# Kernel tuning notes

Hardware: AMD Instinct MI355X
Metric: run time of the kernel (lower is better)

The kernel has to match this reference:

```python
import jax, jax.numpy as jnp
import numpy as np

B, T, U = 4, 256, 128
EH, PH, JH, V = 1024, 640, 640, 1024


def setup_inputs() -> dict:
    key = jax.random.key(0)
    ks = jax.random.split(key, 8)
    s_e = 1.0 / np.sqrt(EH)
    s_p = 1.0 / np.sqrt(PH)
    s_j = 1.0 / np.sqrt(JH)
    return {
        "enc": jax.random.normal(ks[0], (B, EH, T), jnp.float32),
        "dec": jax.random.normal(ks[1], (B, PH, U), jnp.float32),
        "W_enc": jax.random.uniform(ks[2], (JH, EH), jnp.float32, -s_e, s_e),
        "b_enc": jax.random.uniform(ks[3], (JH,), jnp.float32, -s_e, s_e),
        "W_pred": jax.random.uniform(ks[4], (JH, PH), jnp.float32, -s_p, s_p),
        "b_pred": jax.random.uniform(ks[5], (JH,), jnp.float32, -s_p, s_p),
        "W_out": jax.random.uniform(ks[6], (V, JH), jnp.float32, -s_j, s_j),
        "b_out": jax.random.uniform(ks[7], (V,), jnp.float32, -s_j, s_j),
    }


def reference(enc, dec, W_enc, b_enc, W_pred, b_pred, W_out, b_out):
    # enc: [B, EH, T], dec: [B, PH, U]  (channels-first, as in torch forward)
    # enc projection -> [B, T, JH] (transpose fused into einsum)
    e = jnp.einsum('bht,jh->btj', enc, W_enc) + b_enc
    # pred projection -> [B, U, JH]
    p = jnp.einsum('bhu,jh->buj', dec, W_pred) + b_pred
    # broadcast add -> [B, T, U, JH], ReLU, output projection -> [B, T, U, V]
    h = jax.nn.relu(e[:, :, None, :] + p[:, None, :, :])
    logits = jnp.einsum('btuj,vj->btuv', h, W_out) + b_out
    return jax.nn.log_softmax(logits, axis=-1)
```

## Files before the change

kernel.cpp:

```cpp
#include <hip/hip_runtime.h>
#include <hip/hip_bf16.h>
#include <stdint.h>

#define B_ 4
#define T_ 256
#define U_ 128
#define EH_ 1024
#define PH_ 640
#define JH_ 640
#define V_ 1024
#define KT_ 20

typedef short bf16x8 __attribute__((ext_vector_type(8)));
typedef float f32x4 __attribute__((ext_vector_type(4)));
typedef unsigned short u16;

__device__ __forceinline__ u16 f2bf(float f) {
  union { float f; uint32_t u; } v;
  v.f = f;
  uint32_t u = v.u;
  return (u16)((u + 0x7FFFu + ((u >> 16) & 1u)) >> 16);
}

__device__ __forceinline__ uint32_t cvt2(float lo, float hi) {
  uint32_t r;
  asm("v_cvt_pk_bf16_f32 %0, %1, %2" : "=v"(r) : "v"(lo), "v"(hi));
  return r;
}

#define LGKM0  asm volatile("s_waitcnt lgkmcnt(0)" ::: "memory")

__global__ void k_transpose_cvt(const float* __restrict__ in, u16* __restrict__ out,
                                int H, int W) {
  __shared__ float tile[32][33];
  int b = blockIdx.z;
  int h0 = blockIdx.y * 32, w0 = blockIdx.x * 32;
  const float* pin = in + (size_t)b * H * W;
  u16* pout = out + (size_t)b * H * W;
  int lw = threadIdx.x & 31, lh = threadIdx.x >> 5;
#pragma unroll
  for (int i = 0; i < 4; i++) {
    int h = lh + i * 8;
    tile[h][lw] = pin[(size_t)(h0 + h) * W + (w0 + lw)];
  }
  __syncthreads();
#pragma unroll
  for (int i = 0; i < 4; i++) {
    int w = lh + i * 8;
    pout[(size_t)(w0 + w) * H + (h0 + lw)] = f2bf(tile[lw][w]);
  }
}

__global__ void k_prep_w(const float* __restrict__ We, const float* __restrict__ Wp,
                         const float* __restrict__ Wo,
                         u16* __restrict__ WeB, u16* __restrict__ WpB,
                         u16* __restrict__ Wpk) {
  int s = blockIdx.x * 256 + threadIdx.x;
  if (s < 163840) {
    int idx = s * 4;
    float4 v = *(const float4*)(We + idx);
    ushort4 o;
    o.x = f2bf(v.x); o.y = f2bf(v.y); o.z = f2bf(v.z); o.w = f2bf(v.w);
    *(ushort4*)(WeB + idx) = o;
  } else if (s < 266240) {
    int idx = (s - 163840) * 4;
    float4 v = *(const float4*)(Wp + idx);
    ushort4 o;
    o.x = f2bf(v.x); o.y = f2bf(v.y); o.z = f2bf(v.z); o.w = f2bf(v.w);
    *(ushort4*)(WpB + idx) = o;
  } else {
    int q = s - 266240;
    int c = q & 1023;
    int g = (q >> 10) & 3;
    int t = q >> 12;
    const float* src = Wo + (size_t)c * JH_ + t * 32 + g * 8;
    float4 a = *(const float4*)src;
    float4 b2 = *(const float4*)(src + 4);
    ushort4 lo, hi;
    lo.x = f2bf(a.x);  lo.y = f2bf(a.y);  lo.z = f2bf(a.z);  lo.w = f2bf(a.w);
    hi.x = f2bf(b2.x); hi.y = f2bf(b2.y); hi.z = f2bf(b2.z); hi.w = f2bf(b2.w);
    u16* d = Wpk + (size_t)q * 8;
    *(ushort4*)d = lo;
    *(ushort4*)(d + 4) = hi;
  }
}

__global__ void k_proj_gemm(const u16* __restrict__ A, const u16* __restrict__ Bm,
                            const float* __restrict__ bias, float* __restrict__ C,
                            int K, int N, size_t strideA, size_t strideC) {
  __shared__ __align__(16) u16 sA[64 * 64];
  __shared__ __align__(16) u16 sB[64 * 64];
  int bb = blockIdx.z;
  const u16* Ab = A + (size_t)bb * strideA;
  float* Cb = C + (size_t)bb * strideC;
  int m0 = blockIdx.x * 64, n0 = blockIdx.y * 64;
  int tid = threadIdx.x;
  int lane = tid & 63, wid = tid >> 6;

  f32x4 acc[2][2] = {};
  for (int kk = 0; kk < K; kk += 64) {
#pragma unroll
    for (int i = 0; i < 2; i++) {
      int c = tid + i * 256;
      int r = c >> 3, kc = c & 7;
      int s = (r << 3) | (kc ^ (r & 7));
      *(bf16x8*)(sA + s * 8) = *(const bf16x8*)(Ab + (size_t)(m0 + r) * K + kk + kc * 8);
      *(bf16x8*)(sB + s * 8) = *(const bf16x8*)(Bm + (size_t)(n0 + r) * K + kk + kc * 8);
    }
    __syncthreads();
    int wr = (wid >> 1) * 32, wc = (wid & 1) * 32;
    int lr = lane & 15, lk = lane >> 4;
#pragma unroll
    for (int ki = 0; ki < 2; ki++) {
      bf16x8 af[2], bq[2];
#pragma unroll
      for (int mf = 0; mf < 2; mf++) {
        int r = wr + mf * 16 + lr;
        int kc = ki * 4 + lk;
        int s = (r << 3) | (kc ^ (r & 7));
        af[mf] = *(const bf16x8*)(sA + s * 8);
      }
#pragma unroll
      for (int nf = 0; nf < 2; nf++) {
        int r = wc + nf * 16 + lr;
        int kc = ki * 4 + lk;
        int s = (r << 3) | (kc ^ (r & 7));
        bq[nf] = *(const bf16x8*)(sB + s * 8);
      }
#pragma unroll
      for (int mf = 0; mf < 2; mf++)
#pragma unroll
        for (int nf = 0; nf < 2; nf++)
          acc[mf][nf] = __builtin_amdgcn_mfma_f32_16x16x32_bf16(af[mf], bq[nf], acc[mf][nf], 0, 0, 0);
    }
    __syncthreads();
  }
  int wr = (wid >> 1) * 32, wc = (wid & 1) * 32;
  int lr = lane & 15, lq = lane >> 4;
#pragma unroll
  for (int nf = 0; nf < 2; nf++) {
    int n = n0 + wc + nf * 16 + lr;
    float bv = bias[n];
#pragma unroll
    for (int mf = 0; mf < 2; mf++) {
#pragma unroll
      for (int r = 0; r < 4; r++) {
        int m = m0 + wr + mf * 16 + lq * 4 + r;
        Cb[(size_t)m * N + n] = acc[mf][nf][r] + bv;
      }
    }
  }
}

__global__ void k_pack_p2(const float* __restrict__ pBuf, float* __restrict__ pPk) {
  int s = blockIdx.x * 256 + threadIdx.x;
  int bh = s / 10240;
  int rem = s - bh * 10240;
  int g4 = rem >> 6;
  int r = rem & 63;
  int b = bh >> 1, half = bh & 1;
  const float* src = pBuf + ((size_t)(b * 128 + half * 64 + r)) * JH_ + g4 * 4;
  float4 v = *(const float4*)src;
  *(float4*)(pPk + (size_t)s * 4) = v;
}

__global__ __launch_bounds__(512)
void k_fused7(const float* __restrict__ e, const float* __restrict__ pPk,
              const u16* __restrict__ Wpk, const float* __restrict__ bout,
              float* __restrict__ out) {
  __shared__ __align__(16) u16 sA[2][4096];
  __shared__ __align__(16) float sE[JH_];
  __shared__ float redm[512];
  __shared__ float reds[512];

  int bid = blockIdx.x;
  int btile = bid >> 1, half = bid & 1, b = btile >> 8;
  int tid = threadIdx.x, lane = tid & 63, wn = tid >> 6;
  int lr = lane & 15, lk = lane >> 4;
  int ph = (bid % 10) * 2;

  const float* eRow = e + (size_t)btile * JH_;
  const float* pPbase = pPk + ((size_t)(b * 2 + half) * 40960) + wn * 256 + lane * 4;
  const u16* wB = Wpk + ((size_t)lk * 1024 + wn * 128 + lr) * 8;
  float* outB = out + ((size_t)btile * U_ + half * 64) * V_;

  int awr = (wn >> 1) * 512 + lane * 8 + (wn & 1) * 4;

  f32x4 acc[4][8] = {};
  bf16x8 bq[2][8];

  auto tp = [&](int t) { int x = t + ph; return x >= KT_ ? x - KT_ : x; };
  auto loadB = [&](int tph, bf16x8* d) {
#pragma unroll
    for (int nf = 0; nf < 8; nf++)
      d[nf] = *(const bf16x8*)(wB + (size_t)tph * 32768 + nf * 128);
  };
  auto loadp = [&](int tph) { return *(const float4*)(pPbase + tph * 2048); };
  auto build = [&](int slot, int tin, int tph, float4 pv) {
    float4 ev = *(const float4*)(&sE[tph * 32 + wn * 4]);
    uint2 w;
    w.x = cvt2(fmaxf(pv.x + ev.x, 0.f), fmaxf(pv.y + ev.y, 0.f));
    w.y = cvt2(fmaxf(pv.z + ev.z, 0.f), fmaxf(pv.w + ev.w, 0.f));
    *(uint2*)(&sA[slot][tin * 2048 + awr]) = w;
  };

  loadB(tp(0), bq[0]);
  for (int i = tid; i < JH_; i += 512) sE[i] = eRow[i];
  float4 p0  = loadp(tp(0));
  float4 p1  = loadp(tp(1));
  float4 pcA = loadp(tp(2));
  float4 pcB = loadp(tp(3));
  float4 pnA = p0, pnB = p0;
  LGKM0;
  __builtin_amdgcn_s_barrier();
  build(0, 0, tp(0), p0);
  build(0, 1, tp(1), p1);
  LGKM0;
  __builtin_amdgcn_s_barrier();

#pragma unroll
  for (int t = 0; t < KT_; t++) {
    if (t + 1 < KT_) loadB(tp(t + 1), bq[(t + 1) & 1]);
    if ((t & 1) == 0) {
      if (t + 4 < KT_) { pnA = loadp(tp(t + 4)); pnB = loadp(tp(t + 5)); }
      if (t + 2 < KT_) {
        int q1 = ((t >> 1) + 1) & 1;
        build(q1, 0, tp(t + 2), pcA);
        build(q1, 1, tp(t + 3), pcB);
      }
    }
    const u16* Ab = &sA[(t >> 1) & 1][(t & 1) * 2048 + lk * 512];
    bf16x8 af[4];
#pragma unroll
    for (int mf = 0; mf < 4; mf++)
      af[mf] = *(const bf16x8*)(Ab + (mf * 16 + lr) * 8);
    __builtin_amdgcn_s_setprio(1);
#pragma unroll
    for (int mf = 0; mf < 4; mf++)
#pragma unroll
      for (int nf = 0; nf < 8; nf++)
        acc[mf][nf] = __builtin_amdgcn_mfma_f32_16x16x32_bf16(bq[t & 1][nf], af[mf], acc[mf][nf], 0, 0, 0);
    __builtin_amdgcn_s_setprio(0);
    if ((t & 1) && t + 1 < KT_) {
      pcA = pnA; pcB = pnB;
      LGKM0;
      __builtin_amdgcn_s_barrier();
    }
  }

#pragma unroll
  for (int nf = 0; nf < 8; nf++) {
    f32x4 bv = *(const f32x4*)(bout + wn * 128 + nf * 16 + lk * 4);
#pragma unroll
    for (int mf = 0; mf < 4; mf++) acc[mf][nf] += bv;
  }
  float gm[4], lsv[4];
#pragma unroll
  for (int mf = 0; mf < 4; mf++) {
    float m = acc[mf][0][0];
#pragma unroll
    for (int nf = 0; nf < 8; nf++)
#pragma unroll
      for (int j = 0; j < 4; j++) m = fmaxf(m, acc[mf][nf][j]);
    m = fmaxf(m, __shfl_xor(m, 16, 64));
    m = fmaxf(m, __shfl_xor(m, 32, 64));
    gm[mf] = m;
  }
  if (lane < 16) {
#pragma unroll
    for (int mf = 0; mf < 4; mf++) redm[(mf * 16 + lr) * 8 + wn] = gm[mf];
  }
  __syncthreads();
#pragma unroll
  for (int mf = 0; mf < 4; mf++) {
    float m = redm[(mf * 16 + lr) * 8];
#pragma unroll
    for (int w = 1; w < 8; w++) m = fmaxf(m, redm[(mf * 16 + lr) * 8 + w]);
    gm[mf] = m;
  }
#pragma unroll
  for (int mf = 0; mf < 4; mf++) {
    float s = 0.f;
#pragma unroll
    for (int nf = 0; nf < 8; nf++)
#pragma unroll
      for (int j = 0; j < 4; j++) s += __expf(acc[mf][nf][j] - gm[mf]);
    s += __shfl_xor(s, 16, 64);
    s += __shfl_xor(s, 32, 64);
    lsv[mf] = s;
  }
  if (lane < 16) {
#pragma unroll
    for (int mf = 0; mf < 4; mf++) reds[(mf * 16 + lr) * 8 + wn] = lsv[mf];
  }
  __syncthreads();
#pragma unroll
  for (int mf = 0; mf < 4; mf++) {
    float s = reds[(mf * 16 + lr) * 8];
#pragma unroll
    for (int w = 1; w < 8; w++) s += reds[(mf * 16 + lr) * 8 + w];
    lsv[mf] = gm[mf] + __logf(s);
  }

#pragma unroll
  for (int mf = 0; mf < 4; mf++) {
    float* orow = outB + (size_t)(mf * 16 + lr) * V_ + wn * 128 + lk * 4;
#pragma unroll
    for (int nf = 0; nf < 8; nf++) {
      f32x4 v = acc[mf][nf] - lsv[mf];
      *(f32x4*)(orow + nf * 16) = v;
    }
  }
}

extern "C" void kernel_launch(void* const* d_in, const int* in_sizes, int n_in,
                              void* d_out, int out_size, void* d_ws, size_t ws_size,
                              hipStream_t stream) {
  const float* enc    = (const float*)d_in[0];
  const float* dec    = (const float*)d_in[1];
  const float* W_enc  = (const float*)d_in[2];
  const float* b_enc  = (const float*)d_in[3];
  const float* W_pred = (const float*)d_in[4];
  const float* b_pred = (const float*)d_in[5];
  const float* W_out  = (const float*)d_in[6];
  const float* b_out  = (const float*)d_in[7];
  float* out = (float*)d_out;

  char* ws = (char*)d_ws;
  size_t off = 0;
  auto alloc = [&](size_t bytes) {
    void* pp = ws + off;
    off = (off + bytes + 255) & ~(size_t)255;
    return pp;
  };
  u16* encT   = (u16*)alloc((size_t)B_ * T_ * EH_ * 2);
  u16* decT   = (u16*)alloc((size_t)B_ * U_ * PH_ * 2);
  u16* WencB  = (u16*)alloc((size_t)JH_ * EH_ * 2);
  u16* WpredB = (u16*)alloc((size_t)JH_ * PH_ * 2);
  u16* Wpk    = (u16*)alloc((size_t)KT_ * 32768 * 2);
  float* eBuf = (float*)alloc((size_t)B_ * T_ * JH_ * 4);
  float* pBuf = (float*)alloc((size_t)B_ * U_ * JH_ * 4);
  float* pPk  = (float*)alloc((size_t)81920 * 4 * 4);

  k_transpose_cvt<<<dim3(T_ / 32, EH_ / 32, B_), 256, 0, stream>>>(enc, encT, EH_, T_);
  k_transpose_cvt<<<dim3(U_ / 32, PH_ / 32, B_), 256, 0, stream>>>(dec, decT, PH_, U_);
  k_prep_w<<<1360, 256, 0, stream>>>(W_enc, W_pred, W_out, WencB, WpredB, Wpk);
  k_proj_gemm<<<dim3(T_ / 64, JH_ / 64, B_), 256, 0, stream>>>(
      encT, WencB, b_enc, eBuf, EH_, JH_, (size_t)T_ * EH_, (size_t)T_ * JH_);
  k_proj_gemm<<<dim3(U_ / 64, JH_ / 64, B_), 256, 0, stream>>>(
      decT, WpredB, b_pred, pBuf, PH_, JH_, (size_t)U_ * PH_, (size_t)U_ * JH_);
  k_pack_p2<<<320, 256, 0, stream>>>(pBuf, pPk);

  k_fused7<<<B_ * T_ * 2, 512, 0, stream>>>(eBuf, pPk, Wpk, b_out, out);
}
```

Measured before the change: 281.7 us.

## Process both U halves per block and overlap output stores with next prologue

Each block of the fused joint kernel now handles both 64-row halves of U for one (b,t), so the grid is halved. Between the halves it issues the W_out and pred loads for the second half before writing the first half's logits, using a scheduling barrier to keep that order. The aim is to hide the epilogue stores and the prologue load latency, and to reuse the encoder row already in shared memory. The cost is fewer blocks in flight, so latency hiding across the GPU depends more on work inside each block, and register pressure goes up.

```diff
diff --git a/kernel.cpp b/kernel.cpp
--- a/kernel.cpp
+++ b/kernel.cpp
@@ -29,6 +29,7 @@
 }
 
 #define LGKM0  asm volatile("s_waitcnt lgkmcnt(0)" ::: "memory")
+#define SCHEDB __builtin_amdgcn_sched_barrier(0)
 
 __global__ void k_transpose_cvt(const float* __restrict__ in, u16* __restrict__ out,
                                 int H, int W) {
@@ -165,7 +166,7 @@
 }
 
 __global__ __launch_bounds__(512)
-void k_fused7(const float* __restrict__ e, const float* __restrict__ pPk,
+void k_fused8(const float* __restrict__ e, const float* __restrict__ pPk,
               const u16* __restrict__ Wpk, const float* __restrict__ bout,
               float* __restrict__ out) {
   __shared__ __align__(16) u16 sA[2][4096];
@@ -174,19 +175,19 @@
   __shared__ float reds[512];
 
   int bid = blockIdx.x;
-  int btile = bid >> 1, half = bid & 1, b = btile >> 8;
+  int btile = bid, b = btile >> 8;
   int tid = threadIdx.x, lane = tid & 63, wn = tid >> 6;
   int lr = lane & 15, lk = lane >> 4;
   int ph = (bid % 10) * 2;
 
   const float* eRow = e + (size_t)btile * JH_;
-  const float* pPbase = pPk + ((size_t)(b * 2 + half) * 40960) + wn * 256 + lane * 4;
   const u16* wB = Wpk + ((size_t)lk * 1024 + wn * 128 + lr) * 8;
-  float* outB = out + ((size_t)btile * U_ + half * 64) * V_;
 
   int awr = (wn >> 1) * 512 + lane * 8 + (wn & 1) * 4;
 
-  f32x4 acc[4][8] = {};
+  const float* pPbase = pPk + ((size_t)(b * 2) * 40960) + wn * 256 + lane * 4;
+  float* outB = out + ((size_t)btile * U_) * V_;
+
   bf16x8 bq[2][8];
 
   auto tp = [&](int t) { int x = t + ph; return x >= KT_ ? x - KT_ : x; };
@@ -218,97 +219,120 @@
   LGKM0;
   __builtin_amdgcn_s_barrier();
 
-#pragma unroll
-  for (int t = 0; t < KT_; t++) {
-    if (t + 1 < KT_) loadB(tp(t + 1), bq[(t + 1) & 1]);
-    if ((t & 1) == 0) {
-      if (t + 4 < KT_) { pnA = loadp(tp(t + 4)); pnB = loadp(tp(t + 5)); }
-      if (t + 2 < KT_) {
-        int q1 = ((t >> 1) + 1) & 1;
-        build(q1, 0, tp(t + 2), pcA);
-        build(q1, 1, tp(t + 3), pcB);
-      }
-    }
-    const u16* Ab = &sA[(t >> 1) & 1][(t & 1) * 2048 + lk * 512];
-    bf16x8 af[4];
-#pragma unroll
-    for (int mf = 0; mf < 4; mf++)
-      af[mf] = *(const bf16x8*)(Ab + (mf * 16 + lr) * 8);
-    __builtin_amdgcn_s_setprio(1);
-#pragma unroll
-    for (int mf = 0; mf < 4; mf++)
+#pragma unroll 1
+  for (int hu = 0; hu < 2; hu++) {
+    f32x4 acc[4][8] = {};
+#pragma unroll
+    for (int t = 0; t < KT_; t++) {
+      if (t + 1 < KT_) loadB(tp(t + 1), bq[(t + 1) & 1]);
+      if ((t & 1) == 0) {
+        if (t + 4 < KT_) { pnA = loadp(tp(t + 4)); pnB = loadp(tp(t + 5)); }
+        if (t + 2 < KT_) {
+          int q1 = ((t >> 1) + 1) & 1;
+          build(q1, 0, tp(t + 2), pcA);
+          build(q1, 1, tp(t + 3), pcB);
+        }
+      }
+      const u16* Ab = &sA[(t >> 1) & 1][(t & 1) * 2048 + lk * 512];
+      bf16x8 af[4];
+#pragma unroll
+      for (int mf = 0; mf < 4; mf++)
+        af[mf] = *(const bf16x8*)(Ab + (mf * 16 + lr) * 8);
+      __builtin_amdgcn_s_setprio(1);
+#pragma unroll
+      for (int mf = 0; mf < 4; mf++)
+#pragma unroll
+        for (int nf = 0; nf < 8; nf++)
+          acc[mf][nf] = __builtin_amdgcn_mfma_f32_16x16x32_bf16(bq[t & 1][nf], af[mf], acc[mf][nf], 0, 0, 0);
+      __builtin_amdgcn_s_setprio(0);
+      if ((t & 1) && t + 1 < KT_) {
+        pcA = pnA; pcB = pnB;
+        LGKM0;
+        __builtin_amdgcn_s_barrier();
+      }
+    }
+
+#pragma unroll
+    for (int nf = 0; nf < 8; nf++) {
+      f32x4 bv = *(const f32x4*)(bout + wn * 128 + nf * 16 + lk * 4);
+#pragma unroll
+      for (int mf = 0; mf < 4; mf++) acc[mf][nf] += bv;
+    }
+    float gm[4], lsv[4];
+#pragma unroll
+    for (int mf = 0; mf < 4; mf++) {
+      float m = acc[mf][0][0];
 #pragma unroll
       for (int nf = 0; nf < 8; nf++)
-        acc[mf][nf] = __builtin_amdgcn_mfma_f32_16x16x32_bf16(bq[t & 1][nf], af[mf], acc[mf][nf], 0, 0, 0);
-    __builtin_amdgcn_s_setprio(0);
-    if ((t & 1) && t + 1 < KT_) {
-      pcA = pnA; pcB = pnB;
+#pragma unroll
+        for (int j = 0; j < 4; j++) m = fmaxf(m, acc[mf][nf][j]);
+      m = fmaxf(m, __shfl_xor(m, 16, 64));
+      m = fmaxf(m, __shfl_xor(m, 32, 64));
+      gm[mf] = m;
+    }
+    if (lane < 16) {
+#pragma unroll
+      for (int mf = 0; mf < 4; mf++) redm[(mf * 16 + lr) * 8 + wn] = gm[mf];
+    }
+    __syncthreads();
+#pragma unroll
+    for (int mf = 0; mf < 4; mf++) {
+      float m = redm[(mf * 16 + lr) * 8];
+#pragma unroll
+      for (int w = 1; w < 8; w++) m = fmaxf(m, redm[(mf * 16 + lr) * 8 + w]);
+      gm[mf] = m;
+    }
+#pragma unroll
+    for (int mf = 0; mf < 4; mf++) {
+      float s = 0.f;
+#pragma unroll
+      for (int nf = 0; nf < 8; nf++)
+#pragma unroll
+        for (int j = 0; j < 4; j++) s += __expf(acc[mf][nf][j] - gm[mf]);
+      s += __shfl_xor(s, 16, 64);
+      s += __shfl_xor(s, 32, 64);
+      lsv[mf] = s;
+    }
+    if (lane < 16) {
+#pragma unroll
+      for (int mf = 0; mf < 4; mf++) reds[(mf * 16 + lr) * 8 + wn] = lsv[mf];
+    }
+    __syncthreads();
+#pragma unroll
+    for (int mf = 0; mf < 4; mf++) {
+      float s = reds[(mf * 16 + lr) * 8];
+#pragma unroll
+      for (int w = 1; w < 8; w++) s += reds[(mf * 16 + lr) * 8 + w];
+      lsv[mf] = gm[mf] + __logf(s);
+    }
+
+    float* outC = outB;
+    if (hu == 0) {
+      pPbase = pPk + ((size_t)(b * 2 + 1) * 40960) + wn * 256 + lane * 4;
+      outB = out + ((size_t)btile * U_ + 64) * V_;
+      loadB(tp(0), bq[0]);
+      p0  = loadp(tp(0));
+      p1  = loadp(tp(1));
+      pcA = loadp(tp(2));
+      pcB = loadp(tp(3));
+    }
+    SCHEDB;
+
+#pragma unroll
+    for (int mf = 0; mf < 4; mf++) {
+      float* orow = outC + (size_t)(mf * 16 + lr) * V_ + wn * 128 + lk * 4;
+#pragma unroll
+      for (int nf = 0; nf < 8; nf++) {
+        f32x4 v = acc[mf][nf] - lsv[mf];
+        *(f32x4*)(orow + nf * 16) = v;
+      }
+    }
+
+    if (hu == 0) {
+      build(0, 0, tp(0), p0);
+      build(0, 1, tp(1), p1);
       LGKM0;
       __builtin_amdgcn_s_barrier();
-    }
-  }
-
-#pragma unroll
-  for (int nf = 0; nf < 8; nf++) {
-    f32x4 bv = *(const f32x4*)(bout + wn * 128 + nf * 16 + lk * 4);
-#pragma unroll
-    for (int mf = 0; mf < 4; mf++) acc[mf][nf] += bv;
-  }
-  float gm[4], lsv[4];
-#pragma unroll
-  for (int mf = 0; mf < 4; mf++) {
-    float m = acc[mf][0][0];
-#pragma unroll
-    for (int nf = 0; nf < 8; nf++)
-#pragma unroll
-      for (int j = 0; j < 4; j++) m = fmaxf(m, acc[mf][nf][j]);
-    m = fmaxf(m, __shfl_xor(m, 16, 64));
-    m = fmaxf(m, __shfl_xor(m, 32, 64));
-    gm[mf] = m;
-  }
-  if (lane < 16) {
-#pragma unroll
-    for (int mf = 0; mf < 4; mf++) redm[(mf * 16 + lr) * 8 + wn] = gm[mf];
-  }
-  __syncthreads();
-#pragma unroll
-  for (int mf = 0; mf < 4; mf++) {
-    float m = redm[(mf * 16 + lr) * 8];
-#pragma unroll
-    for (int w = 1; w < 8; w++) m = fmaxf(m, redm[(mf * 16 + lr) * 8 + w]);
-    gm[mf] = m;
-  }
-#pragma unroll
-  for (int mf = 0; mf < 4; mf++) {
-    float s = 0.f;
-#pragma unroll
-    for (int nf = 0; nf < 8; nf++)
-#pragma unroll
-      for (int j = 0; j < 4; j++) s += __expf(acc[mf][nf][j] - gm[mf]);
-    s += __shfl_xor(s, 16, 64);
-    s += __shfl_xor(s, 32, 64);
-    lsv[mf] = s;
-  }
-  if (lane < 16) {
-#pragma unroll
-    for (int mf = 0; mf < 4; mf++) reds[(mf * 16 + lr) * 8 + wn] = lsv[mf];
-  }
-  __syncthreads();
-#pragma unroll
-  for (int mf = 0; mf < 4; mf++) {
-    float s = reds[(mf * 16 + lr) * 8];
-#pragma unroll
-    for (int w = 1; w < 8; w++) s += reds[(mf * 16 + lr) * 8 + w];
-    lsv[mf] = gm[mf] + __logf(s);
-  }
-
-#pragma unroll
-  for (int mf = 0; mf < 4; mf++) {
-    float* orow = outB + (size_t)(mf * 16 + lr) * V_ + wn * 128 + lk * 4;
-#pragma unroll
-    for (int nf = 0; nf < 8; nf++) {
-      f32x4 v = acc[mf][nf] - lsv[mf];
-      *(f32x4*)(orow + nf * 16) = v;
     }
   }
 }
@@ -351,5 +375,5 @@
       decT, WpredB, b_pred, pBuf, PH_, JH_, (size_t)U_ * PH_, (size_t)U_ * JH_);
   k_pack_p2<<<320, 256, 0, stream>>>(pBuf, pPk);
 
-  k_fused7<<<B_ * T_ * 2, 512, 0, stream>>>(eBuf, pPk, Wpk, b_out, out);
-}
+  k_fused8<<<B_ * T_, 512, 0, stream>>>(eBuf, pPk, Wpk, b_out, out);
+}
```

New measurement: 428.0 us. 1.52x slower.
